# Kernel tuning notes

Hardware: AMD Instinct MI355X
Metric: run time of the kernel (lower is better)

The kernel has to match this reference:

```python
import jax, jax.numpy as jnp
import numpy as np

HIDDEN = 256
BLUR_RADIUS = 3  # truncate gaussian (std=1.0) at 3 sigma -> 7-tap separable kernel


def _gauss_kernel(std=1.0):
    t = jnp.arange(-BLUR_RADIUS, BLUR_RADIUS + 1, dtype=jnp.float32)
    k = jnp.exp(-0.5 * (t / std) ** 2)
    return k / k.sum()


def _blur_axis(vol, k, axis):
    # vol: [B,D,D,D]; separable 1D conv along `axis` (1..3), SAME padding
    v = jnp.moveaxis(vol, axis, -1)
    shp = v.shape
    v = v.reshape(-1, 1, shp[-1])
    out = jax.lax.conv_general_dilated(v, k.reshape(1, 1, -1), (1,), 'SAME')
    return jnp.moveaxis(out.reshape(shp), -1, axis)


def low_pass_3d(vol, std=1.0):
    k = _gauss_kernel(std).astype(vol.dtype)
    for ax in (1, 2, 3):
        vol = _blur_axis(vol, k, ax)
    return vol


def generate_sphere_points(n, rng):
    phi = rng.uniform(0, 2 * np.pi, n)
    cos_theta = rng.uniform(-1, 1, n)
    theta = np.arccos(cos_theta)
    r = rng.uniform(0, 1, n) ** (1.0 / 3.0)
    return np.stack([r * np.sin(theta) * np.cos(phi),
                     r * np.sin(theta) * np.sin(phi),
                     r * np.cos(theta)], axis=-1)


def setup_inputs() -> dict:
    key = jax.random.key(0)
    B, LAT, V, D = 8, 128, 65536, 128
    ks = list(jax.random.split(key, 16))
    rng = np.random.default_rng(0)

    def siren_first(k, fan_in, fan_out):
        lim = 1.0 / fan_in
        return jax.random.uniform(k, (fan_in, fan_out), jnp.float32, -lim, lim)

    def siren(k, fan_in, fan_out, c=6.0):
        lim = np.sqrt(c / fan_in) / 30.0
        return jax.random.uniform(k, (fan_in, fan_out), jnp.float32, -lim, lim)

    def head(k, fan_in, fan_out):
        # variance_scaling(scale=1/3, mode=fan_out, uniform)
        lim = np.sqrt(3.0 * (1.0 / 3.0) / fan_out)
        return jax.random.uniform(k, (fan_in, fan_out), jnp.float32, -lim, lim)

    inp = {
        'x': jax.random.normal(ks[0], (B, LAT), jnp.float32),
        'w0': siren_first(ks[1], LAT, HIDDEN), 'b0': jnp.zeros((HIDDEN,), jnp.float32),
        'w1': siren(ks[2], HIDDEN, HIDDEN), 'b1': jnp.zeros((HIDDEN,), jnp.float32),
        'w2': siren(ks[3], HIDDEN, HIDDEN), 'b2': jnp.zeros((HIDDEN,), jnp.float32),
        'w3': siren(ks[4], HIDDEN, HIDDEN), 'b3': jnp.zeros((HIDDEN,), jnp.float32),
        'w4': siren(ks[5], HIDDEN, HIDDEN), 'b4': jnp.zeros((HIDDEN,), jnp.float32),
        'wc': head(ks[6], HIDDEN, 3 * V), 'bc': jnp.zeros((3 * V,), jnp.float32),
        'wv': head(ks[7], HIDDEN, V), 'bv': jnp.zeros((V,), jnp.float32),
        'coords0': jnp.asarray(0.25 * (generate_sphere_points(V, rng) + rng.normal(0, 0.1, (V, 3))), jnp.float32),
        'values0': jnp.zeros((V,), jnp.float32),
        'volume_size': D,
    }
    return inp


# corner offsets, ordered as in the original concat: 000,100,010,001,011,101,110,111 (x,y,z)
_OFFSETS = jnp.array([[0, 0, 0], [1, 0, 0], [0, 1, 0], [0, 0, 1],
                      [0, 1, 1], [1, 0, 1], [1, 1, 0], [1, 1, 1]], dtype=jnp.int32)


def reference(x, w0, b0, w1, b1, w2, b2, w3, b3, w4, b4, wc, bc, wv, bv,
              coords0, values0, volume_size):
    B = x.shape[0]
    V = values0.shape[0]
    D = volume_size
    factor = 0.5 * D
    bf = jnp.bfloat16

    # --- SIREN MLP (hidden layers computed in bf16, heads in fp32) ---
    h = jnp.sin(30.0 * (x.astype(bf) @ w0.astype(bf) + b0.astype(bf)))
    for w, b in ((w1, b1), (w2, b2), (w3, b3)):
        h = jnp.sin(h + (h @ w.astype(bf) + b.astype(bf)))
    h = h @ w4.astype(bf) + b4.astype(bf)
    h = h.astype(jnp.float32)

    delta_coords = (h @ wc + bc).reshape(B, V, 3)
    values = jax.nn.relu(values0[None, :] + (h @ wv + bv))  # [B,V]

    coords = factor * (coords0[None] + delta_coords) + factor  # [B,V,3], voxel units

    # --- trilinear splatting ---
    bposf = jnp.floor(coords)
    bposi = bposf.astype(jnp.int32)              # [B,V,3]
    f = coords - bposf                           # fractional part, [B,V,3]
    # weight per corner: prod_d (f_d if offset else 1-f_d) -> [B,V,8]
    w8 = jnp.prod(jnp.where(_OFFSETS[None, None].astype(bool), f[:, :, None, :], 1.0 - f[:, :, None, :]), axis=-1)
    amp = values[:, :, None] * w8                # [B,V,8]
    idx = bposi[:, :, None, :] + _OFFSETS[None, None]  # [B,V,8,3] (x,y,z)
    # linear index with (z,y,x) layout as in original scatter
    lin = (idx[..., 2] * D + idx[..., 1]) * D + idx[..., 0]  # [B,V,8]

    def scatter_one(lin_b, amp_b):
        return jnp.zeros((D * D * D,), jnp.float32).at[lin_b.ravel()].add(amp_b.ravel())

    grids = jax.vmap(scatter_one)(lin, amp).reshape(B, D, D, D)

    # --- gaussian low-pass, std=1.0 ---
    grids = low_pass_3d(grids, std=1.0)
    return grids
```

## Files before the change

kernel.cpp:

```cpp
#include <hip/hip_runtime.h>
#include <hip/hip_bf16.h>

#define DD 128
#define D3 (DD*DD*DD)
#define NB 8
#define NV 65536
#define HID 256
#define LAT 128

#define NBIN 2048
#define NBIN_TOT (NBIN*NB)
#define NMASK 512

__device__ __forceinline__ float rbf(float x) {
    unsigned u = __float_as_uint(x);
    unsigned r = (u + 0x7fffu + ((u >> 16) & 1u)) & 0xFFFF0000u;
    return __uint_as_float(r);
}

template<int K, int MODE>
__global__ __launch_bounds__(1024) void k_layer(
    const float* __restrict__ in, const float* __restrict__ w,
    const float* __restrict__ bias, float* __restrict__ outp)
{
    __shared__ float in_s[NB * K];
    __shared__ float part[16 * 64 * 9];
    const int tid = threadIdx.x;
    for (int i = tid; i < NB * K; i += 1024) in_s[i] = rbf(in[i]);
    __syncthreads();

    const int cl = tid & 63;
    const int ks = tid >> 6;
    const int col = blockIdx.x * 64 + cl;

    float acc[NB];
    #pragma unroll
    for (int b = 0; b < NB; ++b) acc[b] = 0.f;

    const int k0 = ks * (K / 16);
    #pragma unroll 8
    for (int k = k0; k < k0 + K / 16; ++k) {
        float wk = rbf(w[k * HID + col]);
        #pragma unroll
        for (int b = 0; b < NB; ++b) acc[b] = fmaf(in_s[b * K + k], wk, acc[b]);
    }

    float* pp = part + (ks * 64 + cl) * 9;
    #pragma unroll
    for (int b = 0; b < NB; ++b) pp[b] = acc[b];
    __syncthreads();

    if (tid < 512) {
        const int c2 = tid >> 3, b = tid & 7;
        const int gcol = blockIdx.x * 64 + c2;
        float s = 0.f;
        #pragma unroll
        for (int kk = 0; kk < 16; ++kk) s += part[(kk * 64 + c2) * 9 + b];
        float t = rbf(s);
        t = rbf(t + rbf(bias[gcol]));
        if (MODE == 0) {
            t = rbf(30.0f * t);
            t = rbf(sinf(t));
        } else if (MODE == 1) {
            float r = rbf(in_s[b * K + gcol] + t);
            t = rbf(sinf(r));
        }
        outp[b * HID + gcol] = t;
    }
}

#define PSTR 17
__global__ __launch_bounds__(256, 4) void k_heads(
    const float* __restrict__ h4,
    const float* __restrict__ wc, const float* __restrict__ bc,
    const float* __restrict__ wv, const float* __restrict__ bv,
    const float* __restrict__ coords0, const float* __restrict__ values0,
    float4* __restrict__ posval,
    unsigned* __restrict__ zeroBuf)
{
    __shared__ float hsT[HID * NB];
    __shared__ __align__(16) char uni[4 * 64 * PSTR * 4];
    float4 (*buf)[512] = reinterpret_cast<float4(*)[512]>(uni);
    float* part = reinterpret_cast<float*>(uni);

    const int tid = threadIdx.x;
    const int blk = ((blockIdx.x & 7) << 7) + (blockIdx.x >> 3);
    const int p   = tid & 63;
    const int ks  = tid >> 6;

    {
        int zi = blockIdx.x * 256 + tid;
        if (zi < NBIN_TOT + NMASK) zeroBuf[zi] = 0u;
    }

    for (int i = tid; i < NB * HID; i += 256) {
        int b = i >> 8, k = i & 255;
        hsT[k * 8 + b] = h4[b * HID + k];
    }

    const float4* wc4 = reinterpret_cast<const float4*>(wc);
    const float4* wv4 = reinterpret_cast<const float4*>(wv);

    size_t base0, base1, step1;
    {
        int r = tid / 48, c = tid - r * 48;
        base0 = (size_t)((r >> 1) * 64 + (r & 1)) * 49152 + (size_t)blk * 48 + c;
    }
    const float4* src1;
    if (tid < 128) {
        int t1 = tid + 256;
        int r = t1 / 48, c = t1 - r * 48;
        base1 = (size_t)((r >> 1) * 64 + (r & 1)) * 49152 + (size_t)blk * 48 + c;
        src1 = wc4; step1 = 2 * 49152;
    } else {
        int u = tid - 128;
        int r = u >> 4, c = u & 15;
        base1 = (size_t)((r >> 1) * 64 + (r & 1)) * 16384 + (size_t)blk * 16 + c;
        src1 = wv4; step1 = 2 * 16384;
    }
    const size_t step0 = 2 * 49152;
    const int d0 = tid, d1 = tid + 256;

    float acc[4][8];
    #pragma unroll
    for (int c = 0; c < 4; ++c)
        #pragma unroll
        for (int b = 0; b < NB; ++b) acc[c][b] = 0.f;

    const float4* h4v = reinterpret_cast<const float4*>(hsT);

    float4 R0 = wc4[base0];
    float4 R1 = src1[base1];
    buf[0][d0] = R0; buf[0][d1] = R1;
    R0 = wc4[base0 + step0];
    R1 = src1[base1 + step1];
    __syncthreads();

    float4 R0n, R1n;
    for (int s = 0; s < 32; ++s) {
        if (s + 2 < 32) {
            R0n = wc4[base0 + (size_t)(s + 2) * step0];
            R1n = src1[base1 + (size_t)(s + 2) * step1];
        }
        const int bi = s & 1;
        const float* wcsF = reinterpret_cast<const float*>(&buf[bi][0]);
        const float* wvsF = reinterpret_cast<const float*>(&buf[bi][384]);
        #pragma unroll
        for (int j = 0; j < 2; ++j) {
            const int r = ks * 2 + j;
            const int k = ks * 64 + 2 * s + j;
            float c0 = wcsF[r * 192 + 3 * p];
            float c1 = wcsF[r * 192 + 3 * p + 1];
            float c2 = wcsF[r * 192 + 3 * p + 2];
            float vv = wvsF[r * 64 + p];
            float4 hA_ = h4v[k * 2], hB_ = h4v[k * 2 + 1];
            float hb[8] = {hA_.x, hA_.y, hA_.z, hA_.w, hB_.x, hB_.y, hB_.z, hB_.w};
            #pragma unroll
            for (int b = 0; b < NB; ++b) {
                acc[0][b] = fmaf(hb[b], c0, acc[0][b]);
                acc[1][b] = fmaf(hb[b], c1, acc[1][b]);
                acc[2][b] = fmaf(hb[b], c2, acc[2][b]);
                acc[3][b] = fmaf(hb[b], vv, acc[3][b]);
            }
        }
        __syncthreads();
        if (s < 31) {
            buf[bi ^ 1][d0] = R0;
            buf[bi ^ 1][d1] = R1;
            R0 = R0n; R1 = R1n;
            __syncthreads();
        }
    }
    __syncthreads();

    const int bp = ks;
    const int v  = blk * 64 + p;
    const float factor = 0.5f * DD;
    float* pp = part + (ks * 64 + p) * PSTR;

    #pragma unroll
    for (int phase = 0; phase < 2; ++phase) {
        if (phase) __syncthreads();
        #pragma unroll
        for (int q = 0; q < 4; ++q) {
            int b = phase * 4 + q;
            pp[q * 4 + 0] = acc[0][b]; pp[q * 4 + 1] = acc[1][b];
            pp[q * 4 + 2] = acc[2][b]; pp[q * 4 + 3] = acc[3][b];
        }
        __syncthreads();
        {
            const int b = phase * 4 + bp;
            float A0 = 0.f, A1 = 0.f, A2 = 0.f, A3 = 0.f;
            #pragma unroll
            for (int k2 = 0; k2 < 4; ++k2) {
                const float* rp = part + (k2 * 64 + p) * PSTR + bp * 4;
                A0 += rp[0]; A1 += rp[1]; A2 += rp[2]; A3 += rp[3];
            }
            float px = factor * (coords0[3 * v]     + (A0 + bc[3 * v]))     + factor;
            float py = factor * (coords0[3 * v + 1] + (A1 + bc[3 * v + 1])) + factor;
            float pz = factor * (coords0[3 * v + 2] + (A2 + bc[3 * v + 2])) + factor;
            float val = fmaxf(values0[v] + (A3 + bv[v]), 0.f);
            posval[(size_t)b * NV + v] = make_float4(px, py, pz, val);
        }
    }
}

__device__ __forceinline__ bool point_base(float4 q, int& ix, int& iy, int& iz) {
    if (q.w == 0.f) return false;
    ix = (int)floorf(q.x); iy = (int)floorf(q.y); iz = (int)floorf(q.z);
    return ix >= -1 && ix <= 127 && iy >= -1 && iy <= 127 && iz >= -1 && iz <= 127;
}

__device__ __forceinline__ void brick_span(int ix, int iy, int iz,
                                           int& bx0, int& bx1, int& by0, int& by1,
                                           int& bz0, int& bz1) {
    bx0 = (ix < 0 ? 0 : ix) >> 5;  bx1 = (ix + 1 > 127 ? 127 : ix + 1) >> 5;
    by0 = (iy < 0 ? 0 : iy) >> 3;  by1 = (iy + 1 > 127 ? 127 : iy + 1) >> 3;
    bz0 = (iz < 0 ? 0 : iz) >> 2;  bz1 = (iz + 1 > 127 ? 127 : iz + 1) >> 2;
}

__global__ __launch_bounds__(256) void k_count(const float4* __restrict__ posval,
                                               unsigned* __restrict__ binCount,
                                               unsigned* __restrict__ gmask)
{
    __shared__ unsigned hist[NBIN];
    __shared__ unsigned lmask[64];
    const int tid = threadIdx.x;
    const int batch = blockIdx.x >> 5;
    const size_t base = (size_t)batch * NV + (blockIdx.x & 31) * 2048;
    for (int i = tid; i < NBIN; i += 256) hist[i] = 0;
    if (tid < 64) lmask[tid] = 0;
    __syncthreads();
    #pragma unroll
    for (int j = 0; j < 8; ++j) {
        float4 q = posval[base + j * 256 + tid];
        int ix, iy, iz;
        if (point_base(q, ix, iy, iz)) {
            int bx0, bx1, by0, by1, bz0, bz1;
            brick_span(ix, iy, iz, bx0, bx1, by0, by1, bz0, bz1);
            for (int bz = bz0; bz <= bz1; ++bz)
                for (int by = by0; by <= by1; ++by)
                    for (int bx = bx0; bx <= bx1; ++bx)
                        atomicAdd(&hist[(bz * 16 + by) * 4 + bx], 1u);
            int ylo = iy - 3 < 0 ? 0 : iy - 3, yhi = iy + 4 > 127 ? 127 : iy + 4;
            int zlo = iz - 3 < 0 ? 0 : iz - 3, zhi = iz + 4 > 127 ? 127 : iz + 4;
            for (int zc = zlo >> 4; zc <= zhi >> 4; ++zc)
                for (int yc = ylo >> 4; yc <= yhi >> 4; ++yc)
                    lmask[zc * 8 + yc] = 1u;
        }
    }
    __syncthreads();
    for (int i = tid; i < NBIN; i += 256) {
        unsigned c = hist[i];
        if (c) atomicAdd(&binCount[batch * NBIN + i], c);
    }
    if (tid < 64 && lmask[tid]) atomicOr(&gmask[batch * 64 + tid], 1u);
}

__global__ __launch_bounds__(1024) void k_scan(const unsigned* __restrict__ cnt,
                                               unsigned* __restrict__ start,
                                               unsigned* __restrict__ cursor)
{
    __shared__ unsigned partial[1024];
    const int t = threadIdx.x;
    const int base = t * 16;
    unsigned s = 0;
    #pragma unroll
    for (int j = 0; j < 16; ++j) s += cnt[base + j];
    partial[t] = s;
    __syncthreads();
    for (int off = 1; off < 1024; off <<= 1) {
        unsigned mine = partial[t];
        unsigned add = (t >= off) ? partial[t - off] : 0u;
        __syncthreads();
        partial[t] = mine + add;
        __syncthreads();
    }
    unsigned run = (t > 0) ? partial[t - 1] : 0u;
    #pragma unroll
    for (int j = 0; j < 16; ++j) {
        start[base + j] = run;
        cursor[base + j] = run;
        run += cnt[base + j];
    }
    if (t == 1023) start[NBIN_TOT] = partial[1023];
}

__global__ __launch_bounds__(256) void k_scatter(const float4* __restrict__ posval,
                                                 unsigned* __restrict__ binCursor,
                                                 float4* __restrict__ sorted)
{
    __shared__ unsigned hist[NBIN];
    __shared__ unsigned bbase[NBIN];
    const int tid = threadIdx.x;
    const int batch = blockIdx.x >> 5;
    const size_t base = (size_t)batch * NV + (blockIdx.x & 31) * 2048;
    for (int i = tid; i < NBIN; i += 256) hist[i] = 0;
    __syncthreads();

    float4 q[8];
    #pragma unroll
    for (int j = 0; j < 8; ++j) {
        q[j] = posval[base + j * 256 + tid];
        int ix, iy, iz;
        if (point_base(q[j], ix, iy, iz)) {
            int bx0, bx1, by0, by1, bz0, bz1;
            brick_span(ix, iy, iz, bx0, bx1, by0, by1, bz0, bz1);
            for (int bz = bz0; bz <= bz1; ++bz)
                for (int by = by0; by <= by1; ++by)
                    for (int bx = bx0; bx <= bx1; ++bx)
                        atomicAdd(&hist[(bz * 16 + by) * 4 + bx], 1u);
        }
    }
    __syncthreads();
    for (int i = tid; i < NBIN; i += 256) {
        unsigned c = hist[i];
        bbase[i] = c ? atomicAdd(&binCursor[batch * NBIN + i], c) : 0u;
    }
    __syncthreads();
    for (int i = tid; i < NBIN; i += 256) hist[i] = 0;
    __syncthreads();
    #pragma unroll
    for (int j = 0; j < 8; ++j) {
        int ix, iy, iz;
        if (point_base(q[j], ix, iy, iz)) {
            int bx0, bx1, by0, by1, bz0, bz1;
            brick_span(ix, iy, iz, bx0, bx1, by0, by1, bz0, bz1);
            for (int bz = bz0; bz <= bz1; ++bz)
                for (int by = by0; by <= by1; ++by)
                    for (int bx = bx0; bx <= bx1; ++bx) {
                        int bin = (bz * 16 + by) * 4 + bx;
                        unsigned r = atomicAdd(&hist[bin], 1u);
                        sorted[bbase[bin] + r] = q[j];
                    }
        }
    }
}

__global__ __launch_bounds__(256) void k_binsplat(const float4* __restrict__ sorted,
                                                  const unsigned* __restrict__ binStart,
                                                  const unsigned* __restrict__ gmask,
                                                  int maskon,
                                                  float* __restrict__ grid)
{
    __shared__ float brick[4 * 8 * 32];
    const int tid = threadIdx.x;
    const int bid = blockIdx.x;
    const int bx = bid & 3;
    const int by = (bid >> 2) & 15;
    const int bz = (bid >> 6) & 31;
    const int batch = bid >> 11;
    const int x0 = bx << 5, y0 = by << 3, z0 = bz << 2;

    if (maskon && gmask[batch * 64 + (bz >> 2) * 8 + (by >> 1)] == 0u) return;

    const unsigned s = binStart[bid], e = binStart[bid + 1];

    const int vx4 = tid & 7, cy = (tid >> 3) & 7, cz = tid >> 6;
    const size_t o = (size_t)batch * D3 + (size_t)(z0 + cz) * (DD * DD)
                   + (size_t)(y0 + cy) * DD + x0 + vx4 * 4;

    if (s == e) {
        *reinterpret_cast<float4*>(grid + o) = make_float4(0.f, 0.f, 0.f, 0.f);
        return;
    }

    for (int i = tid; i < 1024; i += 256) brick[i] = 0.f;
    __syncthreads();

    for (unsigned i = s + tid; i < e; i += 256) {
        float4 q = sorted[i];
        float fx = floorf(q.x), fy = floorf(q.y), fz = floorf(q.z);
        int vx = (int)fx - x0, vy = (int)fy - y0, vz = (int)fz - z0;
        float gx = q.x - fx, gy = q.y - fy, gz = q.z - fz;
        float wx0 = 1.f - gx, wy0 = 1.f - gy, wz0 = 1.f - gz;
        #pragma unroll
        for (int oz = 0; oz < 2; ++oz)
        #pragma unroll
        for (int oy = 0; oy < 2; ++oy)
        #pragma unroll
        for (int ox = 0; ox < 2; ++ox) {
            int cxx = vx + ox, cyy = vy + oy, czz = vz + oz;
            if ((unsigned)cxx < 32u && (unsigned)cyy < 8u && (unsigned)czz < 4u) {
                float w = ((ox ? gx : wx0) * (oy ? gy : wy0)) * (oz ? gz : wz0);
                atomicAdd(&brick[(czz * 8 + cyy) * 32 + cxx], q.w * w);
            }
        }
    }
    __syncthreads();

    *reinterpret_cast<float4*>(grid + o) =
        *reinterpret_cast<const float4*>(&brick[(cz * 8 + cy) * 32 + vx4 * 4]);
}

__global__ __launch_bounds__(256) void k_blur_z(const float* __restrict__ in,
                                                float* __restrict__ out,
                                                const unsigned* __restrict__ gmask,
                                                int maskon)
{
    const int b = blockIdx.x;
    const int batch = b >> 13;
    const int z = (b >> 6) & 127;
    const int y0 = (b * 2) & 127;
    const long i = (long)b * 256 + threadIdx.x;

    unsigned okbits = 0x7fu;
    if (maskon) {
        if (gmask[batch * 64 + (z >> 4) * 8 + (y0 >> 4)] == 0u) return;
        okbits = 0u;
        #pragma unroll
        for (int j = -3; j <= 3; ++j) {
            int zj = z + j;
            if (zj >= 0 && zj < DD && gmask[batch * 64 + (zj >> 4) * 8 + (y0 >> 4)])
                okbits |= 1u << (j + 3);
        }
    }

    const double e1 = 0.6065306597126334, e2 = 0.1353352832366127, e3 = 0.011108996538242306;
    const double s = 1.0 + 2.0 * (e1 + e2 + e3);
    const float kw[7] = {(float)(e3 / s), (float)(e2 / s), (float)(e1 / s), (float)(1.0 / s),
                         (float)(e1 / s), (float)(e2 / s), (float)(e3 / s)};

    float acc = 0.f;
    #pragma unroll
    for (int j = -3; j <= 3; ++j) {
        int q = z + j;
        if (q >= 0 && q < DD && ((okbits >> (j + 3)) & 1u))
            acc = fmaf(kw[j + 3], in[i + ((long)j << 14)], acc);
    }
    out[i] = acc;
}

__global__ __launch_bounds__(256) void k_blur_yx(const float* __restrict__ in,
                                                 float* __restrict__ out,
                                                 const unsigned* __restrict__ gmask,
                                                 int maskon)
{
    __shared__ float sin_[38 * 128];
    __shared__ float sy[32 * 128];
    __shared__ unsigned mrow[8];

    const double e1 = 0.6065306597126334, e2 = 0.1353352832366127, e3 = 0.011108996538242306;
    const double ss = 1.0 + 2.0 * (e1 + e2 + e3);
    const float kw[7] = {(float)(e3 / ss), (float)(e2 / ss), (float)(e1 / ss), (float)(1.0 / ss),
                         (float)(e1 / ss), (float)(e2 / ss), (float)(e3 / ss)};

    const int tid = threadIdx.x;
    const int bid = blockIdx.x;
    const int ytile = bid & 3;
    const int z = (bid >> 2) & 127;
    const int batch = bid >> 9;
    const int y0 = ytile << 5;
    const size_t slab = (size_t)batch * D3 + (size_t)z * (DD * DD);

    if (maskon) {
        if (tid < 8) mrow[tid] = gmask[batch * 64 + (z >> 4) * 8 + tid];
        __syncthreads();
        const int yc0 = y0 >> 4;
        if (mrow[yc0] == 0u && mrow[yc0 + 1] == 0u) {
            const float4 z4 = make_float4(0.f, 0.f, 0.f, 0.f);
            for (int i = tid; i < 1024; i += 256) {
                int r = i >> 5, xq = i & 31;
                *reinterpret_cast<float4*>(&out[slab + (size_t)(y0 + r) * DD + xq * 4]) = z4;
            }
            return;
        }
    }

    for (int i = tid; i < 38 * 128; i += 256) {
        int row = i >> 7, xx = i & 127;
        int gy = y0 + row - 3;
        bool ok = gy >= 0 && gy < DD && (!maskon || mrow[gy >> 4]);
        sin_[i] = ok ? in[slab + (size_t)gy * DD + xx] : 0.f;
    }
    __syncthreads();

    for (int i = tid; i < 32 * 128; i += 256) {
        int r = i >> 7, xx = i & 127;
        float acc = 0.f;
        #pragma unroll
        for (int j = 0; j < 7; ++j)
            acc = fmaf(kw[j], sin_[(r + j) * 128 + xx], acc);
        sy[i] = acc;
    }
    __syncthreads();

    for (int i = tid; i < 32 * 128; i += 256) {
        int r = i >> 7, xx = i & 127;
        float acc = 0.f;
        #pragma unroll
        for (int j = -3; j <= 3; ++j) {
            int qx = xx + j;
            if (qx >= 0 && qx < DD)
                acc = fmaf(kw[j + 3], sy[r * 128 + qx], acc);
        }
        out[slab + (size_t)(y0 + r) * DD + xx] = acc;
    }
}

extern "C" void kernel_launch(void* const* d_in, const int* in_sizes, int n_in,
                              void* d_out, int out_size, void* d_ws, size_t ws_size,
                              hipStream_t stream) {
    const float* x   = (const float*)d_in[0];
    const float* w0  = (const float*)d_in[1];
    const float* b0  = (const float*)d_in[2];
    const float* w1  = (const float*)d_in[3];
    const float* b1  = (const float*)d_in[4];
    const float* w2  = (const float*)d_in[5];
    const float* b2  = (const float*)d_in[6];
    const float* w3  = (const float*)d_in[7];
    const float* b3  = (const float*)d_in[8];
    const float* w4  = (const float*)d_in[9];
    const float* b4  = (const float*)d_in[10];
    const float* wc  = (const float*)d_in[11];
    const float* bc  = (const float*)d_in[12];
    const float* wv  = (const float*)d_in[13];
    const float* bv  = (const float*)d_in[14];
    const float* c0  = (const float*)d_in[15];
    const float* v0  = (const float*)d_in[16];

    float* out = (float*)d_out;
    float4* posval = (float4*)d_out;
    float* h4 = out + 4 * 1024 * 1024;
    float* hA = h4 + 2048;
    float* hB = hA + 2048;

    const int maskon = (ws_size >= (65ull << 20)) ? 1 : 0;
    const size_t ctrl_off = maskon ? (64ull << 20) : (48ull << 20);
    float4* sorted = (float4*)d_ws;
    unsigned* binCount  = (unsigned*)((char*)d_ws + ctrl_off);
    unsigned* gmask     = binCount + NBIN_TOT;
    unsigned* binStart  = gmask + NMASK;
    unsigned* binCursor = binStart + NBIN_TOT + 1;

    k_layer<LAT, 0><<<4, 1024, 0, stream>>>(x,  w0, b0, hA);
    k_layer<HID, 1><<<4, 1024, 0, stream>>>(hA, w1, b1, hB);
    k_layer<HID, 1><<<4, 1024, 0, stream>>>(hB, w2, b2, hA);
    k_layer<HID, 1><<<4, 1024, 0, stream>>>(hA, w3, b3, hB);
    k_layer<HID, 2><<<4, 1024, 0, stream>>>(hB, w4, b4, h4);

    k_heads<<<NV / 64, 256, 0, stream>>>(h4, wc, bc, wv, bv, c0, v0, posval, binCount);

    k_count<<<256, 256, 0, stream>>>(posval, binCount, gmask);
    k_scan<<<1, 1024, 0, stream>>>(binCount, binStart, binCursor);
    k_scatter<<<256, 256, 0, stream>>>(posval, binCursor, sorted);
    k_binsplat<<<NBIN_TOT, 256, 0, stream>>>(sorted, binStart, gmask, maskon, out);

    const int nblk = (NB * D3) / 256;
    k_blur_z<<<nblk, 256, 0, stream>>>(out, (float*)d_ws, gmask, maskon);
    k_blur_yx<<<NB * 512, 256, 0, stream>>>((float*)d_ws, out, gmask, maskon);
}
```

Measured before the change: 276.3 us.

## Fuse SIREN MLP layers into heads kernel with per-block redundant recompute

Removes the five small per-layer MLP kernels and instead has every k_heads block recompute the full 5-layer MLP for all 8 batch rows in shared memory before running the head GEMM. This eliminates four-plus kernel launches, their serial dependency chain, and the global round-trip of hidden activations. The cost is that each of the 1024 blocks re-reads roughly a megabyte of MLP weights and repeats the same matmuls, adding heavy L2 traffic and a long serialized prologue. The enlarged shared buffer may also reduce occupancy.

```diff
diff --git a/kernel.cpp b/kernel.cpp
--- a/kernel.cpp
+++ b/kernel.cpp
@@ -18,60 +18,14 @@
     return __uint_as_float(r);
 }
 
-template<int K, int MODE>
-__global__ __launch_bounds__(1024) void k_layer(
-    const float* __restrict__ in, const float* __restrict__ w,
-    const float* __restrict__ bias, float* __restrict__ outp)
-{
-    __shared__ float in_s[NB * K];
-    __shared__ float part[16 * 64 * 9];
-    const int tid = threadIdx.x;
-    for (int i = tid; i < NB * K; i += 1024) in_s[i] = rbf(in[i]);
-    __syncthreads();
-
-    const int cl = tid & 63;
-    const int ks = tid >> 6;
-    const int col = blockIdx.x * 64 + cl;
-
-    float acc[NB];
-    #pragma unroll
-    for (int b = 0; b < NB; ++b) acc[b] = 0.f;
-
-    const int k0 = ks * (K / 16);
-    #pragma unroll 8
-    for (int k = k0; k < k0 + K / 16; ++k) {
-        float wk = rbf(w[k * HID + col]);
-        #pragma unroll
-        for (int b = 0; b < NB; ++b) acc[b] = fmaf(in_s[b * K + k], wk, acc[b]);
-    }
-
-    float* pp = part + (ks * 64 + cl) * 9;
-    #pragma unroll
-    for (int b = 0; b < NB; ++b) pp[b] = acc[b];
-    __syncthreads();
-
-    if (tid < 512) {
-        const int c2 = tid >> 3, b = tid & 7;
-        const int gcol = blockIdx.x * 64 + c2;
-        float s = 0.f;
-        #pragma unroll
-        for (int kk = 0; kk < 16; ++kk) s += part[(kk * 64 + c2) * 9 + b];
-        float t = rbf(s);
-        t = rbf(t + rbf(bias[gcol]));
-        if (MODE == 0) {
-            t = rbf(30.0f * t);
-            t = rbf(sinf(t));
-        } else if (MODE == 1) {
-            float r = rbf(in_s[b * K + gcol] + t);
-            t = rbf(sinf(r));
-        }
-        outp[b * HID + gcol] = t;
-    }
-}
-
 #define PSTR 17
 __global__ __launch_bounds__(256, 4) void k_heads(
-    const float* __restrict__ h4,
+    const float* __restrict__ x,
+    const float* __restrict__ w0, const float* __restrict__ b0,
+    const float* __restrict__ w1, const float* __restrict__ b1,
+    const float* __restrict__ w2, const float* __restrict__ b2,
+    const float* __restrict__ w3, const float* __restrict__ b3,
+    const float* __restrict__ w4, const float* __restrict__ b4,
     const float* __restrict__ wc, const float* __restrict__ bc,
     const float* __restrict__ wv, const float* __restrict__ bv,
     const float* __restrict__ coords0, const float* __restrict__ values0,
@@ -79,7 +33,7 @@
     unsigned* __restrict__ zeroBuf)
 {
     __shared__ float hsT[HID * NB];
-    __shared__ __align__(16) char uni[4 * 64 * PSTR * 4];
+    __shared__ __align__(16) char uni[20480];
     float4 (*buf)[512] = reinterpret_cast<float4(*)[512]>(uni);
     float* part = reinterpret_cast<float*>(uni);
 
@@ -91,11 +45,6 @@
     {
         int zi = blockIdx.x * 256 + tid;
         if (zi < NBIN_TOT + NMASK) zeroBuf[zi] = 0u;
-    }
-
-    for (int i = tid; i < NB * HID; i += 256) {
-        int b = i >> 8, k = i & 255;
-        hsT[k * 8 + b] = h4[b * HID + k];
     }
 
     const float4* wc4 = reinterpret_cast<const float4*>(wc);
@@ -121,16 +70,103 @@
     const size_t step0 = 2 * 49152;
     const int d0 = tid, d1 = tid + 256;
 
-    float acc[4][8];
-    #pragma unroll
-    for (int c = 0; c < 4; ++c)
-        #pragma unroll
-        for (int b = 0; b < NB; ++b) acc[c][b] = 0.f;
-
-    const float4* h4v = reinterpret_cast<const float4*>(hsT);
-
     float4 R0 = wc4[base0];
     float4 R1 = src1[base1];
+
+    {
+        float* hbA = reinterpret_cast<float*>(uni);
+        float* hbB = hbA + HID * NB;
+        float* xsT = hbB + HID * NB;
+
+        for (int i = tid; i < NB * LAT; i += 256) {
+            int b = i >> 7, k = i & 127;
+            xsT[k * 8 + b] = rbf(x[i]);
+        }
+        __syncthreads();
+
+        float a[NB];
+        const float4* xsp = reinterpret_cast<const float4*>(xsT);
+
+        #pragma unroll
+        for (int b = 0; b < NB; ++b) a[b] = 0.f;
+        #pragma unroll 8
+        for (int k = 0; k < LAT; ++k) {
+            float wk = rbf(w0[k * HID + tid]);
+            float4 hA_ = xsp[k * 2], hB_ = xsp[k * 2 + 1];
+            float hb[8] = {hA_.x, hA_.y, hA_.z, hA_.w, hB_.x, hB_.y, hB_.z, hB_.w};
+            #pragma unroll
+            for (int b = 0; b < NB; ++b) a[b] = fmaf(hb[b], wk, a[b]);
+        }
+        {
+            float bb = rbf(b0[tid]);
+            #pragma unroll
+            for (int b = 0; b < NB; ++b) {
+                float t = rbf(a[b]);
+                t = rbf(t + bb);
+                t = rbf(30.0f * t);
+                hbA[tid * 8 + b] = rbf(sinf(t));
+            }
+        }
+        __syncthreads();
+
+        const float* Ws[3] = {w1, w2, w3};
+        const float* Bs[3] = {b1, b2, b3};
+        float* cur = hbA;
+        float* nxt = hbB;
+        for (int L = 0; L < 3; ++L) {
+            const float* w = Ws[L];
+            const float4* hp = reinterpret_cast<const float4*>(cur);
+            #pragma unroll
+            for (int b = 0; b < NB; ++b) a[b] = 0.f;
+            #pragma unroll 8
+            for (int k = 0; k < HID; ++k) {
+                float wk = rbf(w[k * HID + tid]);
+                float4 hA_ = hp[k * 2], hB_ = hp[k * 2 + 1];
+                float hb[8] = {hA_.x, hA_.y, hA_.z, hA_.w, hB_.x, hB_.y, hB_.z, hB_.w};
+                #pragma unroll
+                for (int b = 0; b < NB; ++b) a[b] = fmaf(hb[b], wk, a[b]);
+            }
+            float bb = rbf(Bs[L][tid]);
+            #pragma unroll
+            for (int b = 0; b < NB; ++b) {
+                float t = rbf(a[b]);
+                t = rbf(t + bb);
+                float r = rbf(cur[tid * 8 + b] + t);
+                nxt[tid * 8 + b] = rbf(sinf(r));
+            }
+            __syncthreads();
+            float* tmp = cur; cur = nxt; nxt = tmp;
+        }
+        {
+            const float4* hp = reinterpret_cast<const float4*>(cur);
+            #pragma unroll
+            for (int b = 0; b < NB; ++b) a[b] = 0.f;
+            #pragma unroll 8
+            for (int k = 0; k < HID; ++k) {
+                float wk = rbf(w4[k * HID + tid]);
+                float4 hA_ = hp[k * 2], hB_ = hp[k * 2 + 1];
+                float hb[8] = {hA_.x, hA_.y, hA_.z, hA_.w, hB_.x, hB_.y, hB_.z, hB_.w};
+                #pragma unroll
+                for (int b = 0; b < NB; ++b) a[b] = fmaf(hb[b], wk, a[b]);
+            }
+            float bb = rbf(b4[tid]);
+            #pragma unroll
+            for (int b = 0; b < NB; ++b) {
+                float t = rbf(a[b]);
+                hsT[tid * 8 + b] = rbf(t + bb);
+            }
+        }
+        __syncthreads();
+    }
+
+    float acc[4][8];
+    #pragma unroll
+    for (int c = 0; c < 4; ++c)
+        #pragma unroll
+        for (int b = 0; b < NB; ++b) acc[c][b] = 0.f;
+
+    const float4* h4v = reinterpret_cast<const float4*>(hsT);
+
     buf[0][d0] = R0; buf[0][d1] = R1;
     R0 = wc4[base0 + step0];
     R1 = src1[base1 + step1];
@@ -521,9 +557,6 @@
 
     float* out = (float*)d_out;
     float4* posval = (float4*)d_out;
-    float* h4 = out + 4 * 1024 * 1024;
-    float* hA = h4 + 2048;
-    float* hB = hA + 2048;
 
     const int maskon = (ws_size >= (65ull << 20)) ? 1 : 0;
     const size_t ctrl_off = maskon ? (64ull << 20) : (48ull << 20);
@@ -533,13 +566,8 @@
     unsigned* binStart  = gmask + NMASK;
     unsigned* binCursor = binStart + NBIN_TOT + 1;
 
-    k_layer<LAT, 0><<<4, 1024, 0, stream>>>(x,  w0, b0, hA);
-    k_layer<HID, 1><<<4, 1024, 0, stream>>>(hA, w1, b1, hB);
-    k_layer<HID, 1><<<4, 1024, 0, stream>>>(hB, w2, b2, hA);
-    k_layer<HID, 1><<<4, 1024, 0, stream>>>(hA, w3, b3, hB);
-    k_layer<HID, 2><<<4, 1024, 0, stream>>>(hB, w4, b4, h4);
-
-    k_heads<<<NV / 64, 256, 0, stream>>>(h4, wc, bc, wv, bv, c0, v0, posval, binCount);
+    k_heads<<<NV / 64, 256, 0, stream>>>(x, w0, b0, w1, b1, w2, b2, w3, b3, w4, b4,
+                                         wc, bc, wv, bv, c0, v0, posval, binCount);
 
     k_count<<<256, 256, 0, stream>>>(posval, binCount, gmask);
     k_scan<<<1, 1024, 0, stream>>>(binCount, binStart, binCursor);
```

Result: slower. 342.7 us (+24.0%).
